# Performance work log

Hardware: AMD Instinct MI355X
Metric: run time of the kernel (lower is better)

## Reference

```python
import jax, jax.numpy as jnp
import numpy as np

N_SRC = 50000
N_DST = 50000
E = 800000
F_IN = 128
H = 4
D = 32
NEG_SLOPE = 0.2


def setup_inputs() -> dict:
    key = jax.random.key(0)
    k1, k2, k3, k4, k5, k6, k7, k8 = jax.random.split(key, 8)
    src_feat = jax.random.normal(k1, (N_SRC, F_IN), dtype=jnp.float32)
    dst_feat = jax.random.normal(k2, (N_DST, F_IN), dtype=jnp.float32)
    edge_feat = jax.random.normal(k3, (E, F_IN), dtype=jnp.float32)
    src_idx = jax.random.randint(k4, (E,), 0, N_SRC, dtype=jnp.int32)
    dst_idx = jax.random.randint(k5, (E,), 0, N_DST, dtype=jnp.int32)
    # fc_src: in = 2*F_IN (concat op), out = H*D; fc_dst: in = F_IN, out = H*D
    g = np.sqrt(2.0)  # gain for 'relu' (xavier_normal_)
    W_src = jax.random.normal(k6, (2 * F_IN, H * D), dtype=jnp.float32) * (g * np.sqrt(2.0 / (2 * F_IN + H * D)))
    W_dst = jax.random.normal(k7, (F_IN, H * D), dtype=jnp.float32) * (g * np.sqrt(2.0 / (F_IN + H * D)))
    bias = jnp.zeros((H * D,), dtype=jnp.float32)
    return {"src_feat": src_feat, "dst_feat": dst_feat, "edge_feat": edge_feat,
            "W_src": W_src, "W_dst": W_dst, "bias": bias,
            "src_idx": src_idx, "dst_idx": dst_idx}


def reference(src_feat, dst_feat, edge_feat, W_src, W_dst, bias, src_idx, dst_idx):
    # Per-edge message: concat(src[e], edge[e]) @ W_src -> [E, H, D]
    m = jnp.concatenate([src_feat[src_idx], edge_feat], axis=1) @ W_src
    m = m.reshape(E, H, D)
    # Destination projection: [N_dst, H, D]
    nh = (dst_feat @ W_dst).reshape(N_DST, H, D)
    # e_add_v then LeakyReLU -> attention logits [E, H, D]
    scores = jax.nn.leaky_relu(m + nh[dst_idx], negative_slope=NEG_SLOPE)
    # edge_softmax: segment softmax over edges incident to each destination,
    # computed independently per (head, out_feat) channel.
    mx = jax.ops.segment_max(scores, dst_idx, num_segments=N_DST)
    ex = jnp.exp(scores - mx[dst_idx])
    denom = jax.ops.segment_sum(ex, dst_idx, num_segments=N_DST)
    attn = ex / denom[dst_idx]
    # Weighted scatter-add aggregation -> [N_dst, H, D]
    rst = jax.ops.segment_sum(m * attn, dst_idx, num_segments=N_DST)
    rst = rst + bias.reshape(1, H, D)
    return rst
```

## Files before the change

### kernel.cpp

```cpp
#include <hip/hip_runtime.h>


#define F 128
#define C 128
#define NEG 0.2f
#define NN 50000
#define EE 800000

__device__ __forceinline__ void fma4(float4& a, float s, const float4 w) {
    a.x += s * w.x; a.y += s * w.y; a.z += s * w.z; a.w += s * w.w;
}

__global__ __launch_bounds__(256) void node_proj_kernel(
    const float* __restrict__ src_feat, const float* __restrict__ dst_feat,
    const float* __restrict__ W_src, const float* __restrict__ W_dst,
    float* __restrict__ src_proj, float* __restrict__ nh)
{
    const float* in; const float* W; float* out;
    if (blockIdx.y == 0) { in = src_feat; W = W_src; out = src_proj; }
    else                 { in = dst_feat; W = W_dst; out = nh; }

    __shared__ float4 xs[8 * 32];
    const int t  = threadIdx.x;
    const int nb = blockIdx.x * 8;

    {
        int row = t >> 5, col = t & 31;
        xs[t] = ((const float4*)(in + (size_t)(nb + row) * F))[col];
    }
    __syncthreads();

    const int jq = t & 31;
    const int ng = t >> 5;
    float4 acc = make_float4(0.f, 0.f, 0.f, 0.f);
    const float4* W4 = (const float4*)W;

    #pragma unroll 4
    for (int k4 = 0; k4 < 32; ++k4) {
        float4 xv = xs[ng * 32 + k4];
        float4 w0 = W4[(4 * k4 + 0) * 32 + jq];
        float4 w1 = W4[(4 * k4 + 1) * 32 + jq];
        float4 w2 = W4[(4 * k4 + 2) * 32 + jq];
        float4 w3 = W4[(4 * k4 + 3) * 32 + jq];
        fma4(acc, xv.x, w0); fma4(acc, xv.y, w1);
        fma4(acc, xv.z, w2); fma4(acc, xv.w, w3);
    }
    ((float4*)(out + (size_t)(nb + ng) * C))[jq] = acc;
}

__global__ __launch_bounds__(256) void hist_kernel(
    const int* __restrict__ dst_idx, int* __restrict__ deg)
{
    int e = blockIdx.x * 256 + threadIdx.x;
    if (e < EE) atomicAdd(&deg[dst_idx[e]], 1);
}

__global__ __launch_bounds__(1024) void scan_kernel(
    const int* __restrict__ deg, int* __restrict__ cursor)
{
    __shared__ int ssum[1024];
    const int t = threadIdx.x;
    const int chunk = (NN + 1023) / 1024;
    int lo = t * chunk, hi = lo + chunk; if (hi > NN) hi = NN; if (lo > NN) lo = NN;
    int s = 0;
    for (int i = lo; i < hi; ++i) s += deg[i];
    ssum[t] = s;
    __syncthreads();
    for (int d = 1; d < 1024; d <<= 1) {
        int v = (t >= d) ? ssum[t - d] : 0;
        __syncthreads();
        ssum[t] += v;
        __syncthreads();
    }
    int run = ssum[t] - s;
    for (int i = lo; i < hi; ++i) { cursor[i] = run; run += deg[i]; }
}

__global__ __launch_bounds__(256) void scatter_kernel(
    const int* __restrict__ dst_idx, int* __restrict__ cursor, int* __restrict__ elist)
{
    int e = blockIdx.x * 256 + threadIdx.x;
    if (e < EE) {
        int p = atomicAdd(&cursor[dst_idx[e]], 1);
        elist[p] = e;
    }
}

__global__ __launch_bounds__(256) void edge_kernel(
    const float* __restrict__ edge_feat, const float* __restrict__ Wb,
    const float* __restrict__ src_proj, const float* __restrict__ nh,
    const int* __restrict__ src_idx, const int* __restrict__ dst_idx,
    const int* __restrict__ elist,
    float* __restrict__ num, float* __restrict__ den)
{
    __shared__ float4 xs[64 * 32];
    __shared__ int sidx[64];
    __shared__ int didx[64];
    __shared__ int es[64];

    const int t  = threadIdx.x;
    const int eb = blockIdx.x * 64;

    if (t < 64) {
        int e = elist[eb + t];
        es[t] = e;
        sidx[t] = src_idx[e];
        didx[t] = dst_idx[e];
    }
    __syncthreads();

    #pragma unroll
    for (int i = 0; i < 8; ++i) {
        int flat = t + i * 256;
        int row = flat >> 5, col = flat & 31;
        xs[flat] = ((const float4*)(edge_feat + (size_t)es[row] * F))[col];
    }
    __syncthreads();

    const int jq = t & 31;
    const int eg = t >> 5;

    float4 acc[8];
    #pragma unroll
    for (int i = 0; i < 8; ++i) acc[i] = make_float4(0.f, 0.f, 0.f, 0.f);

    const float4* W4 = (const float4*)Wb;

    #pragma unroll 2
    for (int k4 = 0; k4 < 32; ++k4) {
        float4 w0 = W4[(4 * k4 + 0) * 32 + jq];
        float4 w1 = W4[(4 * k4 + 1) * 32 + jq];
        float4 w2 = W4[(4 * k4 + 2) * 32 + jq];
        float4 w3 = W4[(4 * k4 + 3) * 32 + jq];
        #pragma unroll
        for (int i = 0; i < 8; ++i) {
            float4 xv = xs[(eg * 8 + i) * 32 + k4];
            fma4(acc[i], xv.x, w0); fma4(acc[i], xv.y, w1);
            fma4(acc[i], xv.z, w2); fma4(acc[i], xv.w, w3);
        }
    }

    int cur = didx[eg * 8];
    float4 nv = ((const float4*)(nh + (size_t)cur * C))[jq];
    float4 nacc = make_float4(0.f, 0.f, 0.f, 0.f);
    float4 dacc = make_float4(0.f, 0.f, 0.f, 0.f);

    #pragma unroll
    for (int i = 0; i < 8; ++i) {
        int el = eg * 8 + i;
        int d  = didx[el];
        if (d != cur) {
            float* np = num + (size_t)cur * C + jq * 4;
            float* dp = den + (size_t)cur * C + jq * 4;
            atomicAdd(np + 0, nacc.x); atomicAdd(np + 1, nacc.y);
            atomicAdd(np + 2, nacc.z); atomicAdd(np + 3, nacc.w);
            atomicAdd(dp + 0, dacc.x); atomicAdd(dp + 1, dacc.y);
            atomicAdd(dp + 2, dacc.z); atomicAdd(dp + 3, dacc.w);
            nacc = make_float4(0.f, 0.f, 0.f, 0.f);
            dacc = make_float4(0.f, 0.f, 0.f, 0.f);
            cur = d;
            nv = ((const float4*)(nh + (size_t)d * C))[jq];
        }
        float4 sp = ((const float4*)(src_proj + (size_t)sidx[el] * C))[jq];

        float m0 = acc[i].x + sp.x, m1 = acc[i].y + sp.y;
        float m2 = acc[i].z + sp.z, m3 = acc[i].w + sp.w;

        float s0 = m0 + nv.x, s1 = m1 + nv.y, s2 = m2 + nv.z, s3 = m3 + nv.w;
        s0 = s0 > 0.f ? s0 : NEG * s0;
        s1 = s1 > 0.f ? s1 : NEG * s1;
        s2 = s2 > 0.f ? s2 : NEG * s2;
        s3 = s3 > 0.f ? s3 : NEG * s3;

        float e0 = __expf(s0), e1 = __expf(s1), e2 = __expf(s2), e3 = __expf(s3);

        nacc.x += e0 * m0; nacc.y += e1 * m1; nacc.z += e2 * m2; nacc.w += e3 * m3;
        dacc.x += e0;      dacc.y += e1;      dacc.z += e2;      dacc.w += e3;
    }
    {
        float* np = num + (size_t)cur * C + jq * 4;
        float* dp = den + (size_t)cur * C + jq * 4;
        atomicAdd(np + 0, nacc.x); atomicAdd(np + 1, nacc.y);
        atomicAdd(np + 2, nacc.z); atomicAdd(np + 3, nacc.w);
        atomicAdd(dp + 0, dacc.x); atomicAdd(dp + 1, dacc.y);
        atomicAdd(dp + 2, dacc.z); atomicAdd(dp + 3, dacc.w);
    }
}

__global__ __launch_bounds__(256) void finalize_kernel(
    const float* __restrict__ num, const float* __restrict__ den,
    const float* __restrict__ bias, float* __restrict__ out)
{
    int i = blockIdx.x * 256 + threadIdx.x;
    float4 n = ((const float4*)num)[i];
    float4 d = ((const float4*)den)[i];
    float4 b = ((const float4*)bias)[i & 31];
    float4 r;
    r.x = (d.x != 0.f ? n.x / d.x : 0.f) + b.x;
    r.y = (d.y != 0.f ? n.y / d.y : 0.f) + b.y;
    r.z = (d.z != 0.f ? n.z / d.z : 0.f) + b.z;
    r.w = (d.w != 0.f ? n.w / d.w : 0.f) + b.w;
    ((float4*)out)[i] = r;
}

extern "C" void kernel_launch(void* const* d_in, const int* in_sizes, int n_in,
                              void* d_out, int out_size, void* d_ws, size_t ws_size,
                              hipStream_t stream) {
    const float* src_feat  = (const float*)d_in[0];
    const float* dst_feat  = (const float*)d_in[1];
    const float* edge_feat = (const float*)d_in[2];
    const float* W_src     = (const float*)d_in[3];
    const float* W_dst     = (const float*)d_in[4];
    const float* bias      = (const float*)d_in[5];
    const int*   src_idx   = (const int*)d_in[6];
    const int*   dst_idx   = (const int*)d_in[7];
    float* out = (float*)d_out;

    const size_t NODEF = (size_t)NN * C;

    float* ws       = (float*)d_ws;
    float* src_proj = ws;
    float* nh       = ws + NODEF;
    float* den      = ws + 2 * NODEF;
    int*   deg      = (int*)(ws + 3 * NODEF);
    int*   cursor   = deg + NN;
    int*   elist    = cursor + NN;

    float* num = out;

    hipMemsetAsync(num, 0, NODEF * sizeof(float), stream);
    hipMemsetAsync(den, 0, NODEF * sizeof(float), stream);
    hipMemsetAsync(deg, 0, NN * sizeof(int), stream);

    hist_kernel<<<(EE + 255) / 256, 256, 0, stream>>>(dst_idx, deg);
    scan_kernel<<<1, 1024, 0, stream>>>(deg, cursor);
    scatter_kernel<<<(EE + 255) / 256, 256, 0, stream>>>(dst_idx, cursor, elist);

    node_proj_kernel<<<dim3(NN / 8, 2), 256, 0, stream>>>(
        src_feat, dst_feat, W_src, W_dst, src_proj, nh);

    edge_kernel<<<EE / 64, 256, 0, stream>>>(
        edge_feat, W_src + 128 * 128, src_proj, nh, src_idx, dst_idx, elist, num, den);

    finalize_kernel<<<NODEF / 4 / 256, 256, 0, stream>>>(num, den, bias, out);
}
```

Measured before the change: 1.412 ms.

## Rewrite edge kernel as per-destination CSR wavefront using bf16 MFMA

Replaces the edge-tiled fp32 FMA kernel with a CSR kernel in which each wavefront owns half the channels of one destination node. It walks that node's incoming edges in groups of 16 and computes the edge projection with bf16 MFMA 16x16x32, using a weight matrix pre-transposed and converted to bf16. Per-destination sums are reduced in registers and written directly, which removes the float atomics and the memsets of num and den. The risks are the reduced precision of bf16, load imbalance from degree variance, and the serial per-wave staging loop.

```diff
diff --git a/kernel.cpp b/kernel.cpp
--- a/kernel.cpp
+++ b/kernel.cpp
@@ -1,4 +1,5 @@
 #include <hip/hip_runtime.h>
+#include <hip/hip_bf16.h>
 
 
 #define F 128
@@ -7,6 +8,22 @@
 #define NN 50000
 #define EE 800000
 
+typedef short short8 __attribute__((ext_vector_type(8)));
+typedef float f32x4  __attribute__((ext_vector_type(4)));
+
+__device__ ushort g_wt[C * F];
+
+__device__ __forceinline__ ushort f2bf(float x) {
+    __hip_bfloat16 h = __float2bfloat16(x);
+    return *(ushort*)&h;
+}
+
+__global__ __launch_bounds__(256) void prep_wt_kernel(const float* __restrict__ W_src) {
+    int idx = blockIdx.x * 256 + threadIdx.x;
+    int n = idx >> 7, k = idx & 127;
+    g_wt[idx] = f2bf(W_src[(size_t)(128 + k) * C + n]);
+}
+
 __device__ __forceinline__ void fma4(float4& a, float s, const float4 w) {
     a.x += s * w.x; a.y += s * w.y; a.z += s * w.z; a.w += s * w.w;
 }
@@ -23,7 +40,6 @@
     __shared__ float4 xs[8 * 32];
     const int t  = threadIdx.x;
     const int nb = blockIdx.x * 8;
-
     {
         int row = t >> 5, col = t & 31;
         xs[t] = ((const float4*)(in + (size_t)(nb + row) * F))[col];
@@ -86,104 +102,112 @@
     }
 }
 
-__global__ __launch_bounds__(256) void edge_kernel(
-    const float* __restrict__ edge_feat, const float* __restrict__ Wb,
+__global__ __launch_bounds__(256) void csr_edge_kernel(
+    const float* __restrict__ edge_feat,
     const float* __restrict__ src_proj, const float* __restrict__ nh,
-    const int* __restrict__ src_idx, const int* __restrict__ dst_idx,
-    const int* __restrict__ elist,
+    const int* __restrict__ src_idx, const int* __restrict__ elist,
+    const int* __restrict__ deg, const int* __restrict__ cursor,
     float* __restrict__ num, float* __restrict__ den)
 {
-    __shared__ float4 xs[64 * 32];
-    __shared__ int sidx[64];
-    __shared__ int didx[64];
-    __shared__ int es[64];
-
-    const int t  = threadIdx.x;
-    const int eb = blockIdx.x * 64;
-
-    if (t < 64) {
-        int e = elist[eb + t];
-        es[t] = e;
-        sidx[t] = src_idx[e];
-        didx[t] = dst_idx[e];
-    }
-    __syncthreads();
-
+    __shared__ __align__(16) ushort stage[4][16 * 136];
+    __shared__ int sdix[4][16];
+    __shared__ int seid[4][16];
+
+    const int t    = threadIdx.x;
+    const int w    = t >> 6;
+    const int l    = t & 63;
+    const int gw   = blockIdx.x * 4 + w;
+    const int dst  = gw >> 1;
+    const int half = gw & 1;
+    if (dst >= NN) return;
+
+    const int dg    = deg[dst];
+    const int start = cursor[dst] - dg;
+    const int lo    = l & 15;
+    const int q     = l >> 4;
+
+    short8 bfrag[4][4];
     #pragma unroll
-    for (int i = 0; i < 8; ++i) {
-        int flat = t + i * 256;
-        int row = flat >> 5, col = flat & 31;
-        xs[flat] = ((const float4*)(edge_feat + (size_t)es[row] * F))[col];
-    }
-    __syncthreads();
-
-    const int jq = t & 31;
-    const int eg = t >> 5;
-
-    float4 acc[8];
+    for (int tt = 0; tt < 4; ++tt) {
+        int n = half * 64 + tt * 16 + lo;
+        #pragma unroll
+        for (int s = 0; s < 4; ++s)
+            bfrag[tt][s] = *(const short8*)&g_wt[n * F + s * 32 + q * 8];
+    }
+    float nv[4];
     #pragma unroll
-    for (int i = 0; i < 8; ++i) acc[i] = make_float4(0.f, 0.f, 0.f, 0.f);
-
-    const float4* W4 = (const float4*)Wb;
-
-    #pragma unroll 2
-    for (int k4 = 0; k4 < 32; ++k4) {
-        float4 w0 = W4[(4 * k4 + 0) * 32 + jq];
-        float4 w1 = W4[(4 * k4 + 1) * 32 + jq];
-        float4 w2 = W4[(4 * k4 + 2) * 32 + jq];
-        float4 w3 = W4[(4 * k4 + 3) * 32 + jq];
+    for (int tt = 0; tt < 4; ++tt)
+        nv[tt] = nh[(size_t)dst * C + half * 64 + tt * 16 + lo];
+
+    float nsum[4] = {0.f, 0.f, 0.f, 0.f};
+    float dsum[4] = {0.f, 0.f, 0.f, 0.f};
+    ushort* st = stage[w];
+
+    const int passes = (dg + 15) >> 4;
+    for (int p = 0; p < passes; ++p) {
+        const int base = p * 16;
+
+        if (l < 16) {
+            int el = base + l;
+            int e  = (el < dg) ? elist[start + el] : 0;
+            seid[w][l] = e;
+            sdix[w][l] = (el < dg) ? src_idx[e] : 0;
+        }
         #pragma unroll
         for (int i = 0; i < 8; ++i) {
-            float4 xv = xs[(eg * 8 + i) * 32 + k4];
-            fma4(acc[i], xv.x, w0); fma4(acc[i], xv.y, w1);
-            fma4(acc[i], xv.z, w2); fma4(acc[i], xv.w, w3);
+            int qq  = l + 64 * i;
+            int row = qq >> 5, c4 = qq & 31;
+            int el  = base + row;
+            float4 v = make_float4(0.f, 0.f, 0.f, 0.f);
+            if (el < dg)
+                v = ((const float4*)edge_feat)[(size_t)seid[w][row] * 32 + c4];
+            ushort4 b;
+            b.x = f2bf(v.x); b.y = f2bf(v.y); b.z = f2bf(v.z); b.w = f2bf(v.w);
+            *(ushort4*)&st[row * 136 + c4 * 4] = b;
         }
-    }
-
-    int cur = didx[eg * 8];
-    float4 nv = ((const float4*)(nh + (size_t)cur * C))[jq];
-    float4 nacc = make_float4(0.f, 0.f, 0.f, 0.f);
-    float4 dacc = make_float4(0.f, 0.f, 0.f, 0.f);
+        short8 af[4];
+        #pragma unroll
+        for (int s = 0; s < 4; ++s)
+            af[s] = *(const short8*)&st[lo * 136 + s * 32 + q * 8];
+
+        f32x4 acc[4];
+        #pragma unroll
+        for (int tt = 0; tt < 4; ++tt) acc[tt] = (f32x4){0.f, 0.f, 0.f, 0.f};
+        #pragma unroll
+        for (int tt = 0; tt < 4; ++tt)
+            #pragma unroll
+            for (int s = 0; s < 4; ++s)
+                acc[tt] = __builtin_amdgcn_mfma_f32_16x16x32_bf16(
+                              af[s], bfrag[tt][s], acc[tt], 0, 0, 0);
+
+        #pragma unroll
+        for (int tt = 0; tt < 4; ++tt) {
+            int ch = half * 64 + tt * 16 + lo;
+            #pragma unroll
+            for (int r = 0; r < 4; ++r) {
+                int erow = q * 4 + r;
+                int el   = base + erow;
+                if (el < dg) {
+                    int   si = sdix[w][erow];
+                    float m  = acc[tt][r] + src_proj[(size_t)si * C + ch];
+                    float s  = m + nv[tt];
+                    s = s > 0.f ? s : NEG * s;
+                    float ex = __expf(s);
+                    nsum[tt] += ex * m;
+                    dsum[tt] += ex;
+                }
+            }
+        }
+    }
 
     #pragma unroll
-    for (int i = 0; i < 8; ++i) {
-        int el = eg * 8 + i;
-        int d  = didx[el];
-        if (d != cur) {
-            float* np = num + (size_t)cur * C + jq * 4;
-            float* dp = den + (size_t)cur * C + jq * 4;
-            atomicAdd(np + 0, nacc.x); atomicAdd(np + 1, nacc.y);
-            atomicAdd(np + 2, nacc.z); atomicAdd(np + 3, nacc.w);
-            atomicAdd(dp + 0, dacc.x); atomicAdd(dp + 1, dacc.y);
-            atomicAdd(dp + 2, dacc.z); atomicAdd(dp + 3, dacc.w);
-            nacc = make_float4(0.f, 0.f, 0.f, 0.f);
-            dacc = make_float4(0.f, 0.f, 0.f, 0.f);
-            cur = d;
-            nv = ((const float4*)(nh + (size_t)d * C))[jq];
-        }
-        float4 sp = ((const float4*)(src_proj + (size_t)sidx[el] * C))[jq];
-
-        float m0 = acc[i].x + sp.x, m1 = acc[i].y + sp.y;
-        float m2 = acc[i].z + sp.z, m3 = acc[i].w + sp.w;
-
-        float s0 = m0 + nv.x, s1 = m1 + nv.y, s2 = m2 + nv.z, s3 = m3 + nv.w;
-        s0 = s0 > 0.f ? s0 : NEG * s0;
-        s1 = s1 > 0.f ? s1 : NEG * s1;
-        s2 = s2 > 0.f ? s2 : NEG * s2;
-        s3 = s3 > 0.f ? s3 : NEG * s3;
-
-        float e0 = __expf(s0), e1 = __expf(s1), e2 = __expf(s2), e3 = __expf(s3);
-
-        nacc.x += e0 * m0; nacc.y += e1 * m1; nacc.z += e2 * m2; nacc.w += e3 * m3;
-        dacc.x += e0;      dacc.y += e1;      dacc.z += e2;      dacc.w += e3;
-    }
-    {
-        float* np = num + (size_t)cur * C + jq * 4;
-        float* dp = den + (size_t)cur * C + jq * 4;
-        atomicAdd(np + 0, nacc.x); atomicAdd(np + 1, nacc.y);
-        atomicAdd(np + 2, nacc.z); atomicAdd(np + 3, nacc.w);
-        atomicAdd(dp + 0, dacc.x); atomicAdd(dp + 1, dacc.y);
-        atomicAdd(dp + 2, dacc.z); atomicAdd(dp + 3, dacc.w);
+    for (int tt = 0; tt < 4; ++tt) {
+        float n0 = nsum[tt], d0 = dsum[tt];
+        n0 += __shfl_xor(n0, 16); n0 += __shfl_xor(n0, 32);
+        d0 += __shfl_xor(d0, 16); d0 += __shfl_xor(d0, 32);
+        int ch = half * 64 + tt * 16 + lo;
+        if (q == 0)      num[(size_t)dst * C + ch] = n0;
+        else if (q == 1) den[(size_t)dst * C + ch] = d0;
     }
 }
 
@@ -228,10 +252,9 @@
 
     float* num = out;
 
-    hipMemsetAsync(num, 0, NODEF * sizeof(float), stream);
-    hipMemsetAsync(den, 0, NODEF * sizeof(float), stream);
     hipMemsetAsync(deg, 0, NN * sizeof(int), stream);
 
+    prep_wt_kernel<<<64, 256, 0, stream>>>(W_src);
     hist_kernel<<<(EE + 255) / 256, 256, 0, stream>>>(dst_idx, deg);
     scan_kernel<<<1, 1024, 0, stream>>>(deg, cursor);
     scatter_kernel<<<(EE + 255) / 256, 256, 0, stream>>>(dst_idx, cursor, elist);
@@ -239,8 +262,8 @@
     node_proj_kernel<<<dim3(NN / 8, 2), 256, 0, stream>>>(
         src_feat, dst_feat, W_src, W_dst, src_proj, nh);
 
-    edge_kernel<<<EE / 64, 256, 0, stream>>>(
-        edge_feat, W_src + 128 * 128, src_proj, nh, src_idx, dst_idx, elist, num, den);
+    csr_edge_kernel<<<NN / 2, 256, 0, stream>>>(
+        edge_feat, src_proj, nh, src_idx, elist, deg, cursor, num, den);
 
     finalize_kernel<<<NODEF / 4 / 256, 256, 0, stream>>>(num, den, bias, out);
 }
```

Result: slower. 1.515 ms (+7.3%).
